# Performance work log

Measured on AMD Instinct MI355X. Metric: run time of the kernel, lower is better.

## Reference

```python
import jax, jax.numpy as jnp
import numpy as np

NUM_HEADS = 12
WS = 7
LN_EPS = 1e-5


def _layernorm(x, g, b):
    mu = jnp.mean(x, axis=-1, keepdims=True)
    var = jnp.var(x, axis=-1, keepdims=True)
    return (x - mu) * jax.lax.rsqrt(var + LN_EPS) * g + b


def setup_inputs() -> dict:
    key = jax.random.key(0)
    ks = jax.random.split(key, 6)
    B, win_num, n, C = 32, 64, 50, 384
    x = jax.random.normal(ks[0], (B, win_num, n, C), dtype=jnp.float32)
    std = 0.02
    w_qkv = jax.random.normal(ks[1], (3 * C, C), dtype=jnp.float32) * std  # DSA_qkv (no bias)
    w_qk = jax.random.normal(ks[2], (2 * C, C), dtype=jnp.float32) * std   # PSA_qk (no bias)
    ln_g = jnp.ones((C,), dtype=jnp.float32)
    ln_b = jnp.zeros((C,), dtype=jnp.float32)
    w_proj = jax.random.normal(ks[3], (C, C), dtype=jnp.float32) * std
    b_proj = jnp.zeros((C,), dtype=jnp.float32)
    return {"x": x, "H": 56, "W": 56, "w_qkv": w_qkv, "w_qk": w_qk,
            "ln_g": ln_g, "ln_b": ln_b, "w_proj": w_proj, "b_proj": b_proj}


def reference(x, H, W, w_qkv, w_qk, ln_g, ln_b, w_proj, b_proj):
    B, win_num, n, C = x.shape
    h = NUM_HEADS
    d = C // h
    scale = d ** -0.5
    ws = WS
    hg, wg = -(-H // ws), -(-W // ws)

    # ---- DSA: local window attention over (win_size+1) tokens ----
    qkv = (x @ w_qkv.T).reshape(B, win_num, n, 3, h, d)
    q, k, v = jnp.moveaxis(qkv, 3, 0)
    attn = jnp.einsum('bwqhd,bwkhd->bwhqk', q, k) * scale
    attn = jax.nn.softmax(attn, axis=-1)
    out = jnp.einsum('bwhqk,bwkhd->bwqhd', attn, v).reshape(B, win_num, n, C)
    out = out + x

    # split window summary tokens from window contents
    win_tok = out[:, :, 0, :]
    ax = out[:, :, 1:, :]
    win_tok = jax.nn.gelu(_layernorm(win_tok, ln_g, ln_b), approximate=False)

    # ---- PSA: global attention over window tokens ----
    pqk = (win_tok @ w_qk.T).reshape(B, win_num, 2, h, d)
    pq, pk = jnp.moveaxis(pqk, 2, 0)
    pattn = jnp.einsum('bwhd,bvhd->bhwv', pq, pk) * scale
    pattn = jax.nn.softmax(pattn, axis=-1)
    ax_r = ax.reshape(B, win_num, ws * ws, h, d)
    psa = jnp.einsum('bhwv,bvshd->bwshd', pattn, ax_r).reshape(B, win_num, ws * ws, C)
    out = psa + ax

    # ---- window reverse ----
    out = out.reshape(B, hg, wg, ws, ws, C).swapaxes(2, 3).reshape(B, hg * ws, wg * ws, C)
    out = out[:, :H, :W, :].reshape(B, H * W, C)
    return out @ w_proj.T + b_proj
```

## Files before the change

### kernel.cpp

```cpp
#include <hip/hip_runtime.h>
#include <cstdint>
#include <cstddef>

#define B_   32
#define WN   64
#define NT   50
#define C_   384
#define NH   12
#define HD   32
#define SCALE 0.17677669529663687f

typedef float  f32x4  __attribute__((ext_vector_type(4)));
typedef __bf16 bf16x8 __attribute__((ext_vector_type(8)));

__device__ __forceinline__ float bf2f(unsigned short u) {
  union { unsigned int u; float f; } v; v.u = ((unsigned int)u) << 16; return v.f;
}
__device__ __forceinline__ unsigned short f2bf(float f) {
  union { float f; unsigned int u; } v; v.f = f;
  unsigned int r = v.u + 0x7FFFu + ((v.u >> 16) & 1u);
  return (unsigned short)(r >> 16);
}

__device__ __forceinline__ void gload_lds16(const void* g, void* l) {
  __builtin_amdgcn_global_load_lds(
      (const __attribute__((address_space(1))) void*)g,
      (__attribute__((address_space(3))) void*)l, 16, 0, 0);
}

__global__ __launch_bounds__(256) void cvt_bf16_k(const float* __restrict__ src,
                                                  unsigned short* __restrict__ dst,
                                                  int nquad) {
  int i = blockIdx.x * 256 + threadIdx.x;
  if (i < nquad) {
    float4 v = ((const float4*)src)[i];
    ushort4 o;
    o.x = f2bf(v.x); o.y = f2bf(v.y); o.z = f2bf(v.z); o.w = f2bf(v.w);
    ((ushort4*)dst)[i] = o;
  }
}

template<bool OUT_BF16, bool HAS_BIAS>
__global__ __launch_bounds__(256) void gemm128_k(
    const unsigned short* __restrict__ A,
    const unsigned short* __restrict__ W,
    const float* __restrict__ bias,
    void* __restrict__ Out, int M, int N, int K)
{
  __shared__ unsigned short As[128 * 32];
  __shared__ unsigned short Bs[128 * 32];
  const int linear = blockIdx.y * gridDim.x + blockIdx.x;
  const int nwg    = gridDim.x * gridDim.y;
  const int chunk  = nwg >> 3;
  const int wg     = (linear & 7) * chunk + (linear >> 3);
  const int n0 = (wg % gridDim.x) * 128;
  const int m0 = (wg / gridDim.x) * 128;
  const int t  = threadIdx.x;
  const int lane = t & 63, wv = t >> 6;
  const int ln = lane & 15, kq = (lane >> 4) << 3;
  const int wm = (wv >> 1) << 6, wn = (wv & 1) << 6;

  const int row1 = t >> 2;
  const int ce1  = (t & 3) << 3;
  const size_t arow_a = (size_t)(m0 + row1) * K + ce1;
  const size_t arow_b = (size_t)(n0 + row1) * K + ce1;
  unsigned short* lA0 = As + row1 * 32 + ce1;
  unsigned short* lB0 = Bs + row1 * 32 + ce1;

  f32x4 acc[4][4];
#pragma unroll
  for (int i = 0; i < 4; ++i)
#pragma unroll
    for (int j = 0; j < 4; ++j) acc[i][j] = (f32x4){0.f, 0.f, 0.f, 0.f};

  const int nkb = K >> 5;
  for (int kb = 0; kb < nkb; ++kb) {
    const int k0 = kb << 5;
    if (kb) __syncthreads();
    gload_lds16(A + arow_a + k0,                 lA0);
    gload_lds16(A + arow_a + (size_t)64 * K + k0, lA0 + 64 * 32);
    gload_lds16(W + arow_b + k0,                 lB0);
    gload_lds16(W + arow_b + (size_t)64 * K + k0, lB0 + 64 * 32);
    __syncthreads();

    bf16x8 af[4], bf[4];
#pragma unroll
    for (int i = 0; i < 4; ++i) af[i] = *(const bf16x8*)&As[(wm + i * 16 + ln) * 32 + kq];
#pragma unroll
    for (int j = 0; j < 4; ++j) bf[j] = *(const bf16x8*)&Bs[(wn + j * 16 + ln) * 32 + kq];
#pragma unroll
    for (int i = 0; i < 4; ++i)
#pragma unroll
      for (int j = 0; j < 4; ++j)
        acc[i][j] = __builtin_amdgcn_mfma_f32_16x16x32_bf16(af[i], bf[j], acc[i][j], 0, 0, 0);
  }

  const int orow = (lane >> 4) << 2;
#pragma unroll
  for (int i = 0; i < 4; ++i)
#pragma unroll
    for (int j = 0; j < 4; ++j) {
      int gn = n0 + wn + j * 16 + ln;
      float bb = HAS_BIAS ? bias[gn] : 0.f;
#pragma unroll
      for (int r = 0; r < 4; ++r) {
        int gm = m0 + wm + i * 16 + orow + r;
        float v = acc[i][j][r] + bb;
        if (OUT_BF16) ((unsigned short*)Out)[(size_t)gm * N + gn] = f2bf(v);
        else          ((float*)Out)[(size_t)gm * N + gn] = v;
      }
    }
}

template<bool OUT_BF16, bool HAS_BIAS>
__global__ __launch_bounds__(256) void gemm_bf16_k(
    const unsigned short* __restrict__ A,
    const unsigned short* __restrict__ W,
    const float* __restrict__ bias,
    void* __restrict__ Out, int M, int N, int K)
{
  __shared__ unsigned short As[64][40];
  __shared__ unsigned short Bs[64][40];
  const int n0 = blockIdx.x * 64;
  const int m0 = blockIdx.y * 64;
  const int t  = threadIdx.x;
  const int srow = t >> 2;
  const int sseg = (t & 3) << 3;
  const int lane = t & 63;
  const int wv = t >> 6;
  const int wm = (wv >> 1) << 5;
  const int wn = (wv & 1) << 5;
  const int lr = lane & 15;
  const int kq = (lane >> 4) << 3;

  f32x4 acc[2][2] = {{{0.f,0.f,0.f,0.f},{0.f,0.f,0.f,0.f}},
                     {{0.f,0.f,0.f,0.f},{0.f,0.f,0.f,0.f}}};

  const int nkb = K >> 5;
  for (int kb = 0; kb < nkb; ++kb) {
    const int k0 = kb << 5;
    *(uint4*)&As[srow][sseg] = *(const uint4*)(A + (size_t)(m0 + srow) * K + k0 + sseg);
    *(uint4*)&Bs[srow][sseg] = *(const uint4*)(W + (size_t)(n0 + srow) * K + k0 + sseg);
    __syncthreads();
    bf16x8 a0 = *(const bf16x8*)&As[wm + lr][kq];
    bf16x8 a1 = *(const bf16x8*)&As[wm + 16 + lr][kq];
    bf16x8 b0 = *(const bf16x8*)&Bs[wn + lr][kq];
    bf16x8 b1 = *(const bf16x8*)&Bs[wn + 16 + lr][kq];
    acc[0][0] = __builtin_amdgcn_mfma_f32_16x16x32_bf16(a0, b0, acc[0][0], 0, 0, 0);
    acc[0][1] = __builtin_amdgcn_mfma_f32_16x16x32_bf16(a0, b1, acc[0][1], 0, 0, 0);
    acc[1][0] = __builtin_amdgcn_mfma_f32_16x16x32_bf16(a1, b0, acc[1][0], 0, 0, 0);
    acc[1][1] = __builtin_amdgcn_mfma_f32_16x16x32_bf16(a1, b1, acc[1][1], 0, 0, 0);
    __syncthreads();
  }
  const int orow = (lane >> 4) << 2;
#pragma unroll
  for (int i = 0; i < 2; ++i)
#pragma unroll
    for (int j = 0; j < 2; ++j)
#pragma unroll
      for (int r = 0; r < 4; ++r) {
        int gm = m0 + wm + i * 16 + orow + r;
        int gn = n0 + wn + j * 16 + lr;
        float v = acc[i][j][r];
        if (HAS_BIAS) v += bias[gn];
        if (OUT_BF16) ((unsigned short*)Out)[(size_t)gm * N + gn] = f2bf(v);
        else          ((float*)Out)[(size_t)gm * N + gn] = v;
      }
}

__global__ __launch_bounds__(256) void attn_win_k(
    const unsigned short* __restrict__ qkv,
    const unsigned short* __restrict__ xb,
    unsigned short* __restrict__ outA)
{
  const int w = blockIdx.x, b = blockIdx.y;
  const int t = threadIdx.x;
  const int lane = t & 63, wv = t >> 6;
  const int ln = lane & 15, hi = lane >> 4;

  __shared__ unsigned short Qs[64][40];
  __shared__ unsigned short Ks[64][40];
  __shared__ unsigned short Vt[32][72];
  __shared__ unsigned short Ps[64][72];

  const size_t win = (size_t)(b * WN + w);
  const size_t qkvbase = win * NT * 1152;
  const size_t obase = win * NT * C_;

  for (int h = 0; h < NH; ++h) {
    __syncthreads();
    {
      const int n = t >> 2, seg = (t & 3) << 3;
      uint4 qv = {0,0,0,0}, kv = {0,0,0,0}, vv = {0,0,0,0};
      if (n < NT) {
        const unsigned short* p = qkv + qkvbase + (size_t)n * 1152 + h * HD + seg;
        qv = *(const uint4*)p;
        kv = *(const uint4*)(p + C_);
        vv = *(const uint4*)(p + 2 * C_);
      }
      *(uint4*)&Qs[n][seg] = qv;
      *(uint4*)&Ks[n][seg] = kv;
      const unsigned short* vs = (const unsigned short*)&vv;
#pragma unroll
      for (int j = 0; j < 8; ++j) Vt[seg + j][n] = vs[j];
    }
    __syncthreads();

    f32x4 s[4];
    {
      bf16x8 aq = *(const bf16x8*)&Qs[wv * 16 + ln][hi * 8];
#pragma unroll
      for (int nt = 0; nt < 4; ++nt) {
        bf16x8 bk = *(const bf16x8*)&Ks[nt * 16 + ln][hi * 8];
        s[nt] = __builtin_amdgcn_mfma_f32_16x16x32_bf16(aq, bk, (f32x4){0.f,0.f,0.f,0.f}, 0, 0, 0);
      }
    }

#pragma unroll
    for (int r = 0; r < 4; ++r) {
      float m = -1e30f;
#pragma unroll
      for (int nt = 0; nt < 4; ++nt) {
        float val = s[nt][r] * SCALE;
        s[nt][r] = val;
        if (nt * 16 + ln < NT) m = fmaxf(m, val);
      }
#pragma unroll
      for (int o = 1; o < 16; o <<= 1) m = fmaxf(m, __shfl_xor(m, o));
      float e[4]; float sum = 0.f;
#pragma unroll
      for (int nt = 0; nt < 4; ++nt) {
        e[nt] = (nt * 16 + ln < NT) ? __expf(s[nt][r] - m) : 0.f;
        sum += e[nt];
      }
#pragma unroll
      for (int o = 1; o < 16; o <<= 1) sum += __shfl_xor(sum, o);
      float inv = 1.f / sum;
      int q = wv * 16 + hi * 4 + r;
#pragma unroll
      for (int nt = 0; nt < 4; ++nt)
        Ps[q][nt * 16 + ln] = f2bf(e[nt] * inv);
    }

    f32x4 o0 = {0.f,0.f,0.f,0.f}, o1 = {0.f,0.f,0.f,0.f};
#pragma unroll
    for (int kb = 0; kb < 2; ++kb) {
      bf16x8 bp  = *(const bf16x8*)&Ps[wv * 16 + ln][kb * 32 + hi * 8];
      bf16x8 av0 = *(const bf16x8*)&Vt[ln][kb * 32 + hi * 8];
      bf16x8 av1 = *(const bf16x8*)&Vt[16 + ln][kb * 32 + hi * 8];
      o0 = __builtin_amdgcn_mfma_f32_16x16x32_bf16(av0, bp, o0, 0, 0, 0);
      o1 = __builtin_amdgcn_mfma_f32_16x16x32_bf16(av1, bp, o1, 0, 0, 0);
    }

    const int q = wv * 16 + ln;
    if (q < NT) {
      const unsigned short* xr = xb + obase + (size_t)q * C_ + h * HD;
      unsigned short* orow = outA + obase + (size_t)q * C_ + h * HD;
      ushort4 x0 = *(const ushort4*)(xr + hi * 4);
      ushort4 x1 = *(const ushort4*)(xr + 16 + hi * 4);
      ushort4 r0, r1;
      r0.x = f2bf(o0[0] + bf2f(x0.x)); r0.y = f2bf(o0[1] + bf2f(x0.y));
      r0.z = f2bf(o0[2] + bf2f(x0.z)); r0.w = f2bf(o0[3] + bf2f(x0.w));
      r1.x = f2bf(o1[0] + bf2f(x1.x)); r1.y = f2bf(o1[1] + bf2f(x1.y));
      r1.z = f2bf(o1[2] + bf2f(x1.z)); r1.w = f2bf(o1[3] + bf2f(x1.w));
      *(ushort4*)(orow + hi * 4) = r0;
      *(ushort4*)(orow + 16 + hi * 4) = r1;
    }
  }
}

__global__ __launch_bounds__(64) void ln_gelu_k(
    const unsigned short* __restrict__ outA,
    const float* __restrict__ g, const float* __restrict__ beta,
    unsigned short* __restrict__ wt)
{
  const int row = blockIdx.x;
  const int t = threadIdx.x;
  const size_t base = (size_t)row * NT * C_;
  float v[6];
  float s = 0.f, s2 = 0.f;
#pragma unroll
  for (int i = 0; i < 6; ++i) {
    float xv = bf2f(outA[base + t + i * 64]);
    v[i] = xv; s += xv; s2 += xv * xv;
  }
#pragma unroll
  for (int off = 1; off < 64; off <<= 1) {
    s  += __shfl_xor(s, off);
    s2 += __shfl_xor(s2, off);
  }
  const float mu = s * (1.f / 384.f);
  const float var = s2 * (1.f / 384.f) - mu * mu;
  const float rinv = rsqrtf(var + 1e-5f);
#pragma unroll
  for (int i = 0; i < 6; ++i) {
    int c = t + i * 64;
    float y = (v[i] - mu) * rinv * g[c] + beta[c];
    float ge = 0.5f * y * (1.f + erff(y * 0.70710678118654752f));
    wt[(size_t)row * C_ + c] = f2bf(ge);
  }
}

__global__ __launch_bounds__(64) void pool_attn_k(
    const float* __restrict__ pqk, float* __restrict__ pattn)
{
  const int h = blockIdx.x;
  const int b = blockIdx.y;
  const int t = threadIdx.x;
  __shared__ float qs[64][32];
  __shared__ float ks[64][32];
  __shared__ float L[64][64];
  for (int idx = t; idx < 64 * 32; idx += 64) {
    int n = idx >> 5, dd = idx & 31;
    int sw = dd ^ (((n >> 3) & 7) << 2);
    size_t base = ((size_t)(b * WN + n)) * (2 * C_) + h * HD + dd;
    qs[n][sw] = pqk[base];
    ks[n][sw] = pqk[base + C_];
  }
  __syncthreads();
  const int ti = t >> 3, tj = t & 7;
  const int i0 = ti << 3, j0 = tj << 3;
  const int swi = ti << 2, swj = tj << 2;
  {
    float acc[8][8];
#pragma unroll
    for (int r = 0; r < 8; ++r)
#pragma unroll
      for (int c = 0; c < 8; ++c) acc[r][c] = 0.f;
#pragma unroll
    for (int d0 = 0; d0 < 32; d0 += 4) {
      float4 qv[8], kv[8];
#pragma unroll
      for (int r = 0; r < 8; ++r) qv[r] = *(const float4*)&qs[i0 + r][d0 ^ swi];
#pragma unroll
      for (int c = 0; c < 8; ++c) kv[c] = *(const float4*)&ks[j0 + c][d0 ^ swj];
#pragma unroll
      for (int r = 0; r < 8; ++r)
#pragma unroll
        for (int c = 0; c < 8; ++c)
          acc[r][c] += qv[r].x * kv[c].x + qv[r].y * kv[c].y + qv[r].z * kv[c].z + qv[r].w * kv[c].w;
    }
#pragma unroll
    for (int r = 0; r < 8; ++r)
#pragma unroll
      for (int c4 = 0; c4 < 2; ++c4) {
        float4 o;
        o.x = acc[r][c4 * 4 + 0] * SCALE; o.y = acc[r][c4 * 4 + 1] * SCALE;
        o.z = acc[r][c4 * 4 + 2] * SCALE; o.w = acc[r][c4 * 4 + 3] * SCALE;
        *(float4*)&L[i0 + r][(j0 + c4 * 4) ^ swi] = o;
      }
  }
  __syncthreads();
  {
    const int sw = (t >> 3) << 2;
    float m = -1e30f;
    for (int j = 0; j < 64; ++j) m = fmaxf(m, L[t][j ^ sw]);
    float sum = 0.f;
    for (int j = 0; j < 64; ++j) { float e = __expf(L[t][j ^ sw] - m); L[t][j ^ sw] = e; sum += e; }
    float inv = 1.f / sum;
    float* dst = pattn + (((size_t)b * NH + h) * 64 + t) * 64;
    for (int j = 0; j < 64; ++j) dst[j] = L[t][j ^ sw] * inv;
  }
}

__global__ __launch_bounds__(256) void pool_sa_mfma_k(
    const float* __restrict__ pattn,
    const unsigned short* __restrict__ outA,
    unsigned short* __restrict__ Y)
{
  const int tt = blockIdx.x;
  const int h  = blockIdx.y;
  const int b  = blockIdx.z;
  const int t  = threadIdx.x;

  __shared__ unsigned short Ph[64][72];
  __shared__ unsigned short Pl[64][72];
  __shared__ unsigned short AXT[224][72];

  {
    const float4* src = (const float4*)(pattn + ((size_t)b * NH + h) * 4096);
#pragma unroll
    for (int i = 0; i < 4; ++i) {
      int idx = t + i * 256;
      int row = idx >> 4, seg = (idx & 15) << 2;
      float4 p = src[idx];
      float pv[4] = {p.x, p.y, p.z, p.w};
      unsigned short hs[4], ls[4];
#pragma unroll
      for (int e = 0; e < 4; ++e) {
        hs[e] = f2bf(pv[e]);
        ls[e] = f2bf(pv[e] - bf2f(hs[e]));
      }
      ushort4 hv, lv;
      hv.x = hs[0]; hv.y = hs[1]; hv.z = hs[2]; hv.w = hs[3];
      lv.x = ls[0]; lv.y = ls[1]; lv.z = ls[2]; lv.w = ls[3];
      *(ushort4*)&Ph[row][seg] = hv;
      *(ushort4*)&Pl[row][seg] = lv;
    }
  }

  {
    const unsigned short* axb = outA + ((size_t)(b * WN) * NT + 1 + tt * 7) * C_ + h * HD;
    for (int idx = t; idx < 896; idx += 256) {
      int v2 = idx / 28;
      int c  = idx - v2 * 28;
      int v  = v2 << 1;
      int s  = c >> 2, d8 = (c & 3) << 3;
      const unsigned short* p0 = axb + (size_t)v * (NT * C_) + s * C_ + d8;
      uint4 a0 = *(const uint4*)p0;
      uint4 a1 = *(const uint4*)(p0 + NT * C_);
      int cp = ((v2 >> 2) + (c & 7)) & 7;
      int bo = cp * 8 + (v2 & 3) * 2;
      unsigned int aw[4] = {a0.x, a0.y, a0.z, a0.w};
      unsigned int bw[4] = {a1.x, a1.y, a1.z, a1.w};
      int r0 = c << 3;
#pragma unroll
      for (int jj = 0; jj < 4; ++jj) {
        unsigned int w0 = (aw[jj] & 0xffffu) | (bw[jj] << 16);
        unsigned int w1 = (aw[jj] >> 16) | (bw[jj] & 0xffff0000u);
        *(unsigned int*)&AXT[r0 + jj * 2    ][bo] = w0;
        *(unsigned int*)&AXT[r0 + jj * 2 + 1][bo] = w1;
      }
    }
  }
  __syncthreads();

  const int lane = t & 63, wv = t >> 6;
  const int ln = lane & 15, hi = lane >> 4;

  bf16x8 afh[2], afl[2];
#pragma unroll
  for (int kb = 0; kb < 2; ++kb) {
    afh[kb] = *(const bf16x8*)&Ph[wv * 16 + ln][kb * 32 + hi * 8];
    afl[kb] = *(const bf16x8*)&Pl[wv * 16 + ln][kb * 32 + hi * 8];
  }

  const int wbase  = wv * 16 + hi * 4;
  const int whi    = wbase >> 3;
  const int wlo    = wbase & 7;
  const int wchunk = wbase >> 3;
  unsigned short* yb = Y + ((size_t)b * 3136 + ((size_t)whi * 7 + tt) * 56) * C_ + h * HD;

#pragma unroll
  for (int j = 0; j < 14; ++j) {
    const int row = j * 16 + ln;
    const int g = (row >> 3) & 7;
    f32x4 acc = {0.f, 0.f, 0.f, 0.f};
#pragma unroll
    for (int kb = 0; kb < 2; ++kb) {
      bf16x8 bfr = *(const bf16x8*)&AXT[row][((kb * 4 + hi + g) & 7) * 8];
      acc = __builtin_amdgcn_mfma_f32_16x16x32_bf16(afh[kb], bfr, acc, 0, 0, 0);
      acc = __builtin_amdgcn_mfma_f32_16x16x32_bf16(afl[kb], bfr, acc, 0, 0, 0);
    }
    ushort4 rx = *(const ushort4*)&AXT[row][((wchunk + g) & 7) * 8 + (wbase & 7)];
    const unsigned short rr[4] = {rx.x, rx.y, rx.z, rx.w};
    const int sl = row >> 5, d = row & 31;
    unsigned short* yp = yb + (size_t)(wlo * 7 + sl) * C_ + d;
#pragma unroll
    for (int r = 0; r < 4; ++r)
      yp[(size_t)r * 7 * C_] = f2bf(acc[r] + bf2f(rr[r]));
  }
}

extern "C" void kernel_launch(void* const* d_in, const int* in_sizes, int n_in,
                              void* d_out, int out_size, void* d_ws, size_t ws_size,
                              hipStream_t stream)
{
  (void)in_sizes; (void)n_in; (void)out_size; (void)ws_size;
  const float* x      = (const float*)d_in[0];
  const float* w_qkv  = (const float*)d_in[3];
  const float* w_qk   = (const float*)d_in[4];
  const float* ln_g   = (const float*)d_in[5];
  const float* ln_b   = (const float*)d_in[6];
  const float* w_proj = (const float*)d_in[7];
  const float* b_proj = (const float*)d_in[8];
  float* out = (float*)d_out;

  char* ws = (char*)d_ws;
  size_t off = 0;
  auto alloc = [&](size_t bytes) { size_t o = off; off += (bytes + 255) & ~(size_t)255; return o; };
  const size_t M1 = (size_t)B_ * WN * NT;
  const size_t M7 = (size_t)B_ * 3136;
  unsigned short* qkv    = (unsigned short*)(ws + alloc(M1 * 1152 * 2));
  unsigned short* xb     = (unsigned short*)(ws + alloc(M1 * C_ * 2));
  unsigned short* outA   = (unsigned short*)(ws + alloc(M1 * C_ * 2));
  unsigned short* wqkvb  = (unsigned short*)(ws + alloc(1152 * 384 * 2));
  unsigned short* wqkb   = (unsigned short*)(ws + alloc(768 * 384 * 2));
  unsigned short* wprojb = (unsigned short*)(ws + alloc(384 * 384 * 2));
  unsigned short* wt     = (unsigned short*)(ws + alloc(2048 * 384 * 2));
  float* pqk             = (float*)(ws + alloc(2048 * 768 * 4));
  float* pattn           = (float*)(ws + alloc((size_t)B_ * NH * 64 * 64 * 4));
  unsigned short* Y = xb;

  int q;
  q = (int)(M1 * C_ / 4);
  cvt_bf16_k<<<(q + 255) / 256, 256, 0, stream>>>(x, xb, q);
  q = 1152 * 384 / 4;
  cvt_bf16_k<<<(q + 255) / 256, 256, 0, stream>>>(w_qkv, wqkvb, q);
  q = 768 * 384 / 4;
  cvt_bf16_k<<<(q + 255) / 256, 256, 0, stream>>>(w_qk, wqkb, q);
  q = 384 * 384 / 4;
  cvt_bf16_k<<<(q + 255) / 256, 256, 0, stream>>>(w_proj, wprojb, q);

  gemm128_k<true, false><<<dim3(1152 / 128, M1 / 128), 256, 0, stream>>>(
      xb, wqkvb, nullptr, qkv, (int)M1, 1152, 384);
  attn_win_k<<<dim3(WN, B_), 256, 0, stream>>>(qkv, xb, outA);
  ln_gelu_k<<<2048, 64, 0, stream>>>(outA, ln_g, ln_b, wt);
  gemm_bf16_k<false, false><<<dim3(768 / 64, 2048 / 64), 256, 0, stream>>>(
      wt, wqkb, nullptr, pqk, 2048, 768, 384);
  pool_attn_k<<<dim3(NH, B_), 64, 0, stream>>>(pqk, pattn);
  pool_sa_mfma_k<<<dim3(7, NH, B_), 256, 0, stream>>>(pattn, outA, Y);
  gemm128_k<false, true><<<dim3(384 / 128, M7 / 128), 256, 0, stream>>>(
      Y, wprojb, b_proj, out, (int)M7, 384, 384);
}
```

Measured before the change: 689.9 us.

## Double-buffer LDS tiles in GEMM to overlap global loads with MFMA

The GEMM kernel now uses two LDS buffers for the A and W tiles. It issues direct-to-LDS loads for the next K block before running the MFMAs on the current one, with a single waitcnt plus barrier per iteration. This is meant to hide global-memory latency behind compute and drop one of the two barriers per step. The cost is twice the LDS (32 KB per block), which may lower occupancy.

```diff
diff --git a/kernel.cpp b/kernel.cpp
--- a/kernel.cpp
+++ b/kernel.cpp
@@ -47,8 +47,8 @@
     const float* __restrict__ bias,
     void* __restrict__ Out, int M, int N, int K)
 {
-  __shared__ unsigned short As[128 * 32];
-  __shared__ unsigned short Bs[128 * 32];
+  __shared__ unsigned short As[2][128 * 32];
+  __shared__ unsigned short Bs[2][128 * 32];
   const int linear = blockIdx.y * gridDim.x + blockIdx.x;
   const int nwg    = gridDim.x * gridDim.y;
   const int chunk  = nwg >> 3;
@@ -62,10 +62,9 @@
 
   const int row1 = t >> 2;
   const int ce1  = (t & 3) << 3;
+  const int stoff = row1 * 32 + ce1;
   const size_t arow_a = (size_t)(m0 + row1) * K + ce1;
   const size_t arow_b = (size_t)(n0 + row1) * K + ce1;
-  unsigned short* lA0 = As + row1 * 32 + ce1;
-  unsigned short* lB0 = Bs + row1 * 32 + ce1;
 
   f32x4 acc[4][4];
 #pragma unroll
@@ -74,20 +73,46 @@
     for (int j = 0; j < 4; ++j) acc[i][j] = (f32x4){0.f, 0.f, 0.f, 0.f};
 
   const int nkb = K >> 5;
-  for (int kb = 0; kb < nkb; ++kb) {
-    const int k0 = kb << 5;
-    if (kb) __syncthreads();
-    gload_lds16(A + arow_a + k0,                 lA0);
-    gload_lds16(A + arow_a + (size_t)64 * K + k0, lA0 + 64 * 32);
-    gload_lds16(W + arow_b + k0,                 lB0);
-    gload_lds16(W + arow_b + (size_t)64 * K + k0, lB0 + 64 * 32);
-    __syncthreads();
+
+  {
+    gload_lds16(A + arow_a,                  As[0] + stoff);
+    gload_lds16(A + arow_a + (size_t)64 * K, As[0] + stoff + 64 * 32);
+    gload_lds16(W + arow_b,                  Bs[0] + stoff);
+    gload_lds16(W + arow_b + (size_t)64 * K, Bs[0] + stoff + 64 * 32);
+  }
+  asm volatile("s_waitcnt vmcnt(0)" ::: "memory");
+  __builtin_amdgcn_s_barrier();
+
+  int cur = 0;
+  for (int kb = 0; kb < nkb - 1; ++kb) {
+    const int k1 = (kb + 1) << 5;
+    gload_lds16(A + arow_a + k1,                  As[cur ^ 1] + stoff);
+    gload_lds16(A + arow_a + (size_t)64 * K + k1, As[cur ^ 1] + stoff + 64 * 32);
+    gload_lds16(W + arow_b + k1,                  Bs[cur ^ 1] + stoff);
+    gload_lds16(W + arow_b + (size_t)64 * K + k1, Bs[cur ^ 1] + stoff + 64 * 32);
 
     bf16x8 af[4], bf[4];
 #pragma unroll
-    for (int i = 0; i < 4; ++i) af[i] = *(const bf16x8*)&As[(wm + i * 16 + ln) * 32 + kq];
-#pragma unroll
-    for (int j = 0; j < 4; ++j) bf[j] = *(const bf16x8*)&Bs[(wn + j * 16 + ln) * 32 + kq];
+    for (int i = 0; i < 4; ++i) af[i] = *(const bf16x8*)&As[cur][(wm + i * 16 + ln) * 32 + kq];
+#pragma unroll
+    for (int j = 0; j < 4; ++j) bf[j] = *(const bf16x8*)&Bs[cur][(wn + j * 16 + ln) * 32 + kq];
+#pragma unroll
+    for (int i = 0; i < 4; ++i)
+#pragma unroll
+      for (int j = 0; j < 4; ++j)
+        acc[i][j] = __builtin_amdgcn_mfma_f32_16x16x32_bf16(af[i], bf[j], acc[i][j], 0, 0, 0);
+
+    asm volatile("s_waitcnt vmcnt(0)" ::: "memory");
+    __builtin_amdgcn_s_barrier();
+    cur ^= 1;
+  }
+
+  {
+    bf16x8 af[4], bf[4];
+#pragma unroll
+    for (int i = 0; i < 4; ++i) af[i] = *(const bf16x8*)&As[cur][(wm + i * 16 + ln) * 32 + kq];
+#pragma unroll
+    for (int j = 0; j < 4; ++j) bf[j] = *(const bf16x8*)&Bs[cur][(wn + j * 16 + ln) * 32 + kq];
 #pragma unroll
     for (int i = 0; i < 4; ++i)
 #pragma unroll
```

New measurement: 697.4 us. Within noise of the previous version (+1.1%).

## Double-buffer LDS tiles in bf16 GEMM to overlap global loads with MFMA

Applied to the files above, without the earlier changes.

Turns the shared-memory A/B tiles of the 128x128 GEMM into two-stage buffers and prefetches the k-block two steps ahead with direct global-to-LDS loads. Explicit vmcnt/lgkmcnt waits plus raw barriers replace the two __syncthreads per iteration, so the loads for later k-blocks run while MFMAs execute on the current one. This doubles LDS use per block, which may lower occupancy, and depends on correct hand-written waitcnt ordering. It speeds up only the GEMM parts (QKV and output projection) of the whole pipeline.

```diff
diff --git a/kernel.cpp b/kernel.cpp
--- a/kernel.cpp
+++ b/kernel.cpp
@@ -47,8 +47,8 @@
     const float* __restrict__ bias,
     void* __restrict__ Out, int M, int N, int K)
 {
-  __shared__ unsigned short As[128 * 32];
-  __shared__ unsigned short Bs[128 * 32];
+  __shared__ unsigned short As[2][128 * 32];
+  __shared__ unsigned short Bs[2][128 * 32];
   const int linear = blockIdx.y * gridDim.x + blockIdx.x;
   const int nwg    = gridDim.x * gridDim.y;
   const int chunk  = nwg >> 3;
@@ -62,10 +62,10 @@
 
   const int row1 = t >> 2;
   const int ce1  = (t & 3) << 3;
-  const size_t arow_a = (size_t)(m0 + row1) * K + ce1;
-  const size_t arow_b = (size_t)(n0 + row1) * K + ce1;
-  unsigned short* lA0 = As + row1 * 32 + ce1;
-  unsigned short* lB0 = Bs + row1 * 32 + ce1;
+  const int stoff = row1 * 32 + ce1;
+  const unsigned short* gA = A + (size_t)(m0 + row1) * K + ce1;
+  const unsigned short* gB = W + (size_t)(n0 + row1) * K + ce1;
+  const size_t hstep = (size_t)64 * K;
 
   f32x4 acc[4][4];
 #pragma unroll
@@ -74,25 +74,47 @@
     for (int j = 0; j < 4; ++j) acc[i][j] = (f32x4){0.f, 0.f, 0.f, 0.f};
 
   const int nkb = K >> 5;
+
+  gload_lds16(gA,              As[0] + stoff);
+  gload_lds16(gA + hstep,      As[0] + stoff + 64 * 32);
+  gload_lds16(gB,              Bs[0] + stoff);
+  gload_lds16(gB + hstep,      Bs[0] + stoff + 64 * 32);
+  gload_lds16(gA + 32,         As[1] + stoff);
+  gload_lds16(gA + hstep + 32, As[1] + stoff + 64 * 32);
+  gload_lds16(gB + 32,         Bs[1] + stoff);
+  gload_lds16(gB + hstep + 32, Bs[1] + stoff + 64 * 32);
+  asm volatile("s_waitcnt vmcnt(4)" ::: "memory");
+  __builtin_amdgcn_s_barrier();
+
   for (int kb = 0; kb < nkb; ++kb) {
-    const int k0 = kb << 5;
-    if (kb) __syncthreads();
-    gload_lds16(A + arow_a + k0,                 lA0);
-    gload_lds16(A + arow_a + (size_t)64 * K + k0, lA0 + 64 * 32);
-    gload_lds16(W + arow_b + k0,                 lB0);
-    gload_lds16(W + arow_b + (size_t)64 * K + k0, lB0 + 64 * 32);
-    __syncthreads();
-
+    const int cur = kb & 1;
     bf16x8 af[4], bf[4];
 #pragma unroll
-    for (int i = 0; i < 4; ++i) af[i] = *(const bf16x8*)&As[(wm + i * 16 + ln) * 32 + kq];
-#pragma unroll
-    for (int j = 0; j < 4; ++j) bf[j] = *(const bf16x8*)&Bs[(wn + j * 16 + ln) * 32 + kq];
+    for (int i = 0; i < 4; ++i) af[i] = *(const bf16x8*)&As[cur][(wm + i * 16 + ln) * 32 + kq];
+#pragma unroll
+    for (int j = 0; j < 4; ++j) bf[j] = *(const bf16x8*)&Bs[cur][(wn + j * 16 + ln) * 32 + kq];
+    asm volatile("s_waitcnt lgkmcnt(0)" ::: "memory");
+    __builtin_amdgcn_s_barrier();
+
+    if (kb + 2 < nkb) {
+      const int ko = (kb + 2) << 5;
+      gload_lds16(gA + ko,         As[cur] + stoff);
+      gload_lds16(gA + hstep + ko, As[cur] + stoff + 64 * 32);
+      gload_lds16(gB + ko,         Bs[cur] + stoff);
+      gload_lds16(gB + hstep + ko, Bs[cur] + stoff + 64 * 32);
+    }
+
 #pragma unroll
     for (int i = 0; i < 4; ++i)
 #pragma unroll
       for (int j = 0; j < 4; ++j)
         acc[i][j] = __builtin_amdgcn_mfma_f32_16x16x32_bf16(af[i], bf[j], acc[i][j], 0, 0, 0);
+
+    if (kb + 1 < nkb) {
+      if (kb + 2 < nkb) asm volatile("s_waitcnt vmcnt(4)" ::: "memory");
+      else              asm volatile("s_waitcnt vmcnt(0)" ::: "memory");
+      __builtin_amdgcn_s_barrier();
+    }
   }
 
   const int orow = (lane >> 4) << 2;
```

Result: no change. 690.2 us (+0.0%).
